# Kernel optimization log

Measured on AMD Instinct MI355X. Metric: run time of the kernel, lower is better.

## Reference

```python
import jax, jax.numpy as jnp
import numpy as np

B, S, D, H = 2, 2048, 1024, 16
HD = D // H  # 64
SCALE = float(np.sqrt(HD))


def setup_inputs() -> dict:
    key = jax.random.key(0)
    ks = jax.random.split(key, 5)
    x = jax.random.normal(ks[0], (B, S, D), dtype=jnp.float32)
    # causal mask: 1 = attend, 0 = masked
    mask = jnp.tril(jnp.ones((S, S), dtype=jnp.int32))
    xavier = lambda k: jax.random.normal(k, (D, D), dtype=jnp.float32) * np.sqrt(2.0 / (D + D))
    return {
        "x": x,
        "mask": mask,
        "Wq": xavier(ks[1]),
        "Wk": xavier(ks[2]),
        "Wv": xavier(ks[3]),
        "Wo": xavier(ks[4]),
    }


def reference(x, mask, Wq, Wk, Wv, Wo):
    # torch Linear(bias=False): y = x @ W.T  with W of shape [out, in]
    def heads(W):
        return (x @ W.T).reshape(B, S, H, HD).transpose(0, 2, 1, 3)  # [B,H,S,HD]

    Q, K, V = heads(Wq), heads(Wk), heads(Wv)
    scores = jnp.einsum("bhqd,bhkd->bhqk", Q, K) / SCALE  # [B,H,S,S]
    scores = jnp.where(mask[None, None] == 0, -jnp.inf, scores)
    attn = jax.nn.softmax(scores, axis=-1)
    attn = jnp.where(jnp.isnan(attn), jnp.zeros_like(attn), attn)  # nan-fix for fully masked rows
    # dropout is identity in eval / p=0
    out = jnp.einsum("bhqk,bhkd->bhqd", attn, V)  # [B,H,S,HD]
    out = out.transpose(0, 2, 1, 3).reshape(B, S, D)
    return out @ Wo.T
```

## Files before the change

kernel.cpp:

```cpp
#include <hip/hip_runtime.h>


using bfx8 = __attribute__((ext_vector_type(8))) short;
using fx4  = __attribute__((ext_vector_type(4))) float;

#define NB 2
#define NS 2048
#define ND 1024
#define NH 16
#define NHD 64

__device__ __forceinline__ unsigned short f2bf(float f) {
  union { float f; unsigned u; } v; v.f = f;
  return (unsigned short)((v.u + 0x7fffu + ((v.u >> 16) & 1u)) >> 16);
}
__device__ __forceinline__ unsigned pk2(float a, float b) {
  return (unsigned)f2bf(a) | ((unsigned)f2bf(b) << 16);
}
__device__ __forceinline__ unsigned pkt(float a, float b) {
  union { float f; unsigned u; } ua, ub; ua.f = a; ub.f = b;
  return (ua.u >> 16) | (ub.u & 0xffff0000u);
}
__device__ __forceinline__ int vperm32(int k5) {
  return (((k5 & 15) >> 2) << 3) + (((k5 >> 4) & 1) << 2) + (k5 & 3);
}

#define GLD16(gp, lp) __builtin_amdgcn_global_load_lds( \
    (__attribute__((address_space(1))) void*)(gp),      \
    (__attribute__((address_space(3))) void*)(lp), 16, 0, 0)

__global__ __launch_bounds__(256)
void cvt_all(const float4* __restrict__ x,  const float4* __restrict__ wq,
             const float4* __restrict__ wk, const float4* __restrict__ wv,
             const float4* __restrict__ wo, unsigned short* __restrict__ dst) {
  const int NT4 = (NB * NS * ND) / 4, NW4 = (ND * ND) / 4;
  const int i = blockIdx.x * 256 + threadIdx.x;
  const float4* src;
  int off;
  if (i < NT4) {
    src = x; off = i;
  } else {
    const int k = i - NT4;
    const int seg = k / NW4;
    off = k - seg * NW4;
    src = (seg == 0) ? wq : (seg == 1) ? wk : (seg == 2) ? wv : wo;
  }
  float4 f = src[off];
  uint2 w;
  w.x = pk2(f.x, f.y);
  w.y = pk2(f.z, f.w);
  *(uint2*)(dst + (size_t)i * 4) = w;
}

__global__ __launch_bounds__(256)
void gemm_qkvT(const unsigned short* __restrict__ Wcat,
               const unsigned short* __restrict__ xb,
               unsigned short* __restrict__ Qb, unsigned short* __restrict__ Kb,
               unsigned short* __restrict__ Vt, float SCL) {
  __shared__ __attribute__((aligned(16))) unsigned short As[3][128 * 32];
  __shared__ __attribute__((aligned(16))) unsigned short Bs[3][128 * 32];
  const int t = threadIdx.x;
  const int lane = t & 63, wave = t >> 6;
  const int wr = wave >> 1, wc = wave & 1;
  const int r16 = lane & 15, quad = lane >> 4;
  const int n0 = blockIdx.x * 128;
  const int m0 = blockIdx.y * 128;
  const int KD = 1024;
  fx4 acc[4][4] = {};
  const int c0 = t, c1 = t + 256;
  const size_t a0 = (size_t)(n0 + (c0 >> 2)) * KD + (size_t)(((c0 & 3) ^ ((c0 >> 3) & 3)) * 8);
  const size_t a1 = (size_t)(n0 + (c1 >> 2)) * KD + (size_t)(((c1 & 3) ^ ((c1 >> 3) & 3)) * 8);
  const size_t b0 = (size_t)(m0 + (c0 >> 2)) * KD + (size_t)(((c0 & 3) ^ ((c0 >> 3) & 3)) * 8);
  const size_t b1 = (size_t)(m0 + (c1 >> 2)) * KD + (size_t)(((c1 & 3) ^ ((c1 >> 3) & 3)) * 8);

#define QKVT_STAGE(bi, kk) do {                      \
    GLD16(Wcat + a0 + (kk), &As[bi][c0 * 8]);        \
    GLD16(Wcat + a1 + (kk), &As[bi][c1 * 8]);        \
    GLD16(xb   + b0 + (kk), &Bs[bi][c0 * 8]);        \
    GLD16(xb   + b1 + (kk), &Bs[bi][c1 * 8]);        \
  } while (0)

  QKVT_STAGE(0, 0);
  QKVT_STAGE(1, 32);
  QKVT_STAGE(2, 64);
  const int swr = (quad ^ ((r16 >> 1) & 3)) * 8;
  int cur = 0;
  for (int k0 = 0; k0 < KD; k0 += 32) {
    asm volatile("s_waitcnt vmcnt(8)" ::: "memory");
    __builtin_amdgcn_s_barrier();
    bfx8 af[4], bfr[4];
#pragma unroll
    for (int ni = 0; ni < 4; ni++)
      af[ni] = *(const bfx8*)&As[cur][(wr * 64 + ni * 16 + r16) * 32 + swr];
#pragma unroll
    for (int mi = 0; mi < 4; mi++)
      bfr[mi] = *(const bfx8*)&Bs[cur][(wc * 64 + mi * 16 + r16) * 32 + swr];
#pragma unroll
    for (int ni = 0; ni < 4; ni++)
#pragma unroll
      for (int mi = 0; mi < 4; mi++)
        acc[ni][mi] = __builtin_amdgcn_mfma_f32_16x16x32_bf16(
            af[ni], bfr[mi], acc[ni][mi], 0, 0, 0);
    __builtin_amdgcn_s_barrier();
    int kn = k0 + 96;
    if (kn >= KD) kn = KD - 32;
    QKVT_STAGE(cur, kn);
    cur = (cur == 2) ? 0 : cur + 1;
  }
#undef QKVT_STAGE
#pragma unroll
  for (int ni = 0; ni < 4; ni++) {
#pragma unroll
    for (int mi = 0; mi < 4; mi++) {
      fx4 v = acc[ni][mi];
      const int n = n0 + wr * 64 + ni * 16 + quad * 4;
      const int m = m0 + wc * 64 + mi * 16 + r16;
      const int b = m >> 11, s = m & (NS - 1);
      if (n0 < 1024) {
        const int h = n >> 6, hd = n & (NHD - 1);
        const size_t base = ((size_t)(b * NH + h) * NS + s) * NHD + hd;
        uint2 pw;
        pw.x = pk2(v[0] * SCL, v[1] * SCL);
        pw.y = pk2(v[2] * SCL, v[3] * SCL);
        *(uint2*)(Qb + base) = pw;
      } else if (n0 < 2048) {
        const int n2 = n - 1024;
        const int h = n2 >> 6, hd = n2 & (NHD - 1);
        const size_t base = ((size_t)(b * NH + h) * NS + s) * NHD + hd;
        uint2 pw;
        pw.x = pk2(v[0], v[1]);
        pw.y = pk2(v[2], v[3]);
        *(uint2*)(Kb + base) = pw;
      } else {
        const int n2 = n - 2048;
        const int h = n2 >> 6, hd = n2 & (NHD - 1);
        const int sp = (s & ~31) | vperm32(s & 31);
        const size_t base = ((size_t)(b * NH + h) * NHD + hd) * NS + sp;
#pragma unroll
        for (int r = 0; r < 4; r++) Vt[base + (size_t)r * NS] = f2bf(v[r]);
      }
    }
  }
}

__global__ __launch_bounds__(256)
void gemm_qkv_f32(const float* __restrict__ x,
                  const float* __restrict__ W0, const float* __restrict__ W1,
                  const float* __restrict__ W2,
                  unsigned short* __restrict__ Qb, unsigned short* __restrict__ Kb,
                  unsigned short* __restrict__ Vt, float SCL) {
  __shared__ __attribute__((aligned(16))) unsigned short As[128 * 32];
  __shared__ __attribute__((aligned(16))) unsigned short Bs[128 * 32];
  const int t = threadIdx.x;
  const int lane = t & 63, wave = t >> 6;
  const int wr = wave >> 1, wc = wave & 1;
  const int r16 = lane & 15, quad = lane >> 4;
  const int m0 = blockIdx.x * 128, n0 = blockIdx.y * 128;
  const int z = blockIdx.z;
  const float* W = (z == 0) ? W0 : (z == 1) ? W1 : W2;
  const int KD = 1024;
  fx4 acc[4][4] = {};
  const int row2 = t >> 1, kh = t & 1;
  for (int k0 = 0; k0 < KD; k0 += 32) {
    {
      const float4* src = (const float4*)(x + (size_t)(m0 + row2) * KD + k0 + kh * 16);
      float4 f0 = src[0], f1 = src[1], f2 = src[2], f3 = src[3];
      uint4 w0 = {pk2(f0.x, f0.y), pk2(f0.z, f0.w), pk2(f1.x, f1.y), pk2(f1.z, f1.w)};
      uint4 w1 = {pk2(f2.x, f2.y), pk2(f2.z, f2.w), pk2(f3.x, f3.y), pk2(f3.z, f3.w)};
      *(uint4*)&As[row2 * 32 + kh * 16] = w0;
      *(uint4*)&As[row2 * 32 + kh * 16 + 8] = w1;
    }
    {
      const float4* src = (const float4*)(W + (size_t)(n0 + row2) * KD + k0 + kh * 16);
      float4 f0 = src[0], f1 = src[1], f2 = src[2], f3 = src[3];
      uint4 w0 = {pk2(f0.x, f0.y), pk2(f0.z, f0.w), pk2(f1.x, f1.y), pk2(f1.z, f1.w)};
      uint4 w1 = {pk2(f2.x, f2.y), pk2(f2.z, f2.w), pk2(f3.x, f3.y), pk2(f3.z, f3.w)};
      *(uint4*)&Bs[row2 * 32 + kh * 16] = w0;
      *(uint4*)&Bs[row2 * 32 + kh * 16 + 8] = w1;
    }
    __syncthreads();
    bfx8 af[4], bfr[4];
#pragma unroll
    for (int mt = 0; mt < 4; mt++)
      af[mt] = *(const bfx8*)&As[(wr * 64 + mt * 16 + r16) * 32 + quad * 8];
#pragma unroll
    for (int nt = 0; nt < 4; nt++)
      bfr[nt] = *(const bfx8*)&Bs[(wc * 64 + nt * 16 + r16) * 32 + quad * 8];
#pragma unroll
    for (int mt = 0; mt < 4; mt++)
#pragma unroll
      for (int nt = 0; nt < 4; nt++)
        acc[mt][nt] = __builtin_amdgcn_mfma_f32_16x16x32_bf16(
            af[mt], bfr[nt], acc[mt][nt], 0, 0, 0);
    __syncthreads();
  }
#pragma unroll
  for (int mt = 0; mt < 4; mt++) {
#pragma unroll
    for (int nt = 0; nt < 4; nt++) {
      fx4 v = acc[mt][nt];
      const int mb = m0 + wr * 64 + mt * 16 + quad * 4;
      const int n = n0 + wc * 64 + nt * 16 + r16;
      const int b = mb >> 11, s = mb & (NS - 1);
      const int h = n >> 6, hd = n & (NHD - 1);
      if (z <= 1) {
        unsigned short* C = (z == 0) ? Qb : Kb;
        const float sc = (z == 0) ? SCL : 1.0f;
        const size_t base = ((size_t)(b * NH + h) * NS + s) * NHD + hd;
#pragma unroll
        for (int r = 0; r < 4; r++) C[base + (size_t)r * NHD] = f2bf(v[r] * sc);
      } else {
        const int sp = (s & ~31) | (((s & 15) >> 2) << 3) | (((s >> 4) & 1) << 2);
        const size_t base = ((size_t)(b * NH + h) * NHD + hd) * NS + sp;
        uint2 pw;
        pw.x = pk2(v[0], v[1]);
        pw.y = pk2(v[2], v[3]);
        *(uint2*)(Vt + base) = pw;
      }
    }
  }
}

template <bool BF16>
__global__ __launch_bounds__(256)
void gemm_out(const unsigned short* __restrict__ A,
              const void* __restrict__ Wv,
              float* __restrict__ C) {
  __shared__ __attribute__((aligned(16))) unsigned short As[64 * 64];
  __shared__ __attribute__((aligned(16))) unsigned short Bs[128 * 64];
  const int t = threadIdx.x;
  const int lane = t & 63, wave = t >> 6;
  const int wr = wave >> 1, wc = wave & 1;
  const int r16 = lane & 15, quad = lane >> 4;
  const int m0 = blockIdx.x * 64, n0 = blockIdx.y * 128;
  const int KD = 1024;
  fx4 acc[2][4] = {};
  for (int k0 = 0; k0 < KD; k0 += 64) {
#pragma unroll
    for (int cc = 0; cc < 2; cc++) {
      const int c = t + cc * 256;
      GLD16(A + (size_t)(m0 + (c >> 3)) * KD + (size_t)(((c & 7) ^ ((c >> 3) & 7)) * 8) + k0,
            &As[c * 8]);
    }
    if constexpr (BF16) {
      const unsigned short* W = (const unsigned short*)Wv;
#pragma unroll
      for (int cc = 0; cc < 4; cc++) {
        const int c = t + cc * 256;
        GLD16(W + (size_t)(n0 + (c >> 3)) * KD + (size_t)(((c & 7) ^ ((c >> 3) & 7)) * 8) + k0,
              &Bs[c * 8]);
      }
    } else {
      const float* W = (const float*)Wv;
#pragma unroll
      for (int cc = 0; cc < 4; cc++) {
        const int c = t + cc * 256;
        const float4* src = (const float4*)(W + (size_t)(n0 + (c >> 3)) * KD +
                                            ((c & 7) ^ ((c >> 3) & 7)) * 8 + k0);
        float4 f0 = src[0], f1 = src[1];
        uint4 w0 = {pk2(f0.x, f0.y), pk2(f0.z, f0.w), pk2(f1.x, f1.y), pk2(f1.z, f1.w)};
        *(uint4*)&Bs[c * 8] = w0;
      }
    }
    __syncthreads();
    bfx8 af[2][2], bfr[4][2];
#pragma unroll
    for (int ks = 0; ks < 2; ks++) {
      const int sw = ((ks * 4 + quad) ^ (r16 & 7)) * 8;
#pragma unroll
      for (int mt = 0; mt < 2; mt++)
        af[mt][ks] = *(const bfx8*)&As[(wr * 32 + mt * 16 + r16) * 64 + sw];
#pragma unroll
      for (int nt = 0; nt < 4; nt++)
        bfr[nt][ks] = *(const bfx8*)&Bs[(wc * 64 + nt * 16 + r16) * 64 + sw];
    }
#pragma unroll
    for (int ks = 0; ks < 2; ks++)
#pragma unroll
      for (int mt = 0; mt < 2; mt++)
#pragma unroll
        for (int nt = 0; nt < 4; nt++)
          acc[mt][nt] = __builtin_amdgcn_mfma_f32_16x16x32_bf16(
              af[mt][ks], bfr[nt][ks], acc[mt][nt], 0, 0, 0);
    __syncthreads();
  }
#pragma unroll
  for (int mt = 0; mt < 2; mt++) {
#pragma unroll
    for (int nt = 0; nt < 4; nt++) {
      fx4 v = acc[mt][nt];
      const int s = m0 + wr * 32 + mt * 16 + quad * 4;
      const int n = n0 + wc * 64 + nt * 16 + r16;
      const size_t base = (size_t)s * ND + n;
#pragma unroll
      for (int r = 0; r < 4; r++) C[base + (size_t)r * ND] = v[r];
    }
  }
}

__global__ __launch_bounds__(256)
void attn_mfma(const unsigned short* __restrict__ Q,
               const unsigned short* __restrict__ K,
               const unsigned short* __restrict__ Vt,
               unsigned short* __restrict__ O) {
  __shared__ __attribute__((aligned(16))) unsigned short Ks[64 * 64];
  __shared__ __attribute__((aligned(16))) unsigned short Vs[64 * 64];
  const int t = threadIdx.x;
  const int lane = t & 63, wave = t >> 6;
  const int r16 = lane & 15, quad = lane >> 4;
  const int bh = blockIdx.x;
  const int tile = (gridDim.y - 1) - blockIdx.y;
  const int b = bh >> 4, h = bh & (NH - 1);
  const int q0b = tile * 64;
  const int qbase = q0b + r16 * 4 + wave;
  const int nT = tile + 1;
  const unsigned short* Qp = Q + (size_t)bh * NS * NHD;
  const unsigned short* Kp = K + (size_t)bh * NS * NHD;
  const unsigned short* Vp = Vt + (size_t)bh * NHD * NS;

  bfx8 qf[2];
#pragma unroll
  for (int hs = 0; hs < 2; hs++)
    qf[hs] = *(const bfx8*)&Qp[(size_t)qbase * NHD + hs * 32 + quad * 8];

  fx4 acc[4] = {};
  float lsum = 0.0f;

  const int c0 = t, c1 = t + 256;
  const int ls0 = (c0 >> 3) * 64 + (((c0 & 7) ^ ((c0 >> 3) & 7)) * 8);
  const int ls1 = (c1 >> 3) * 64 + (((c1 & 7) ^ ((c1 >> 3) & 7)) * 8);
  const int rx = r16 & 7;
  uint4 kr0 = *(const uint4*)&Kp[8 * c0];
  uint4 kr1 = *(const uint4*)&Kp[8 * c1];
  uint4 vr0 = *(const uint4*)&Vp[(size_t)(c0 >> 3) * NS + (c0 & 7) * 8];
  uint4 vr1 = *(const uint4*)&Vp[(size_t)(c1 >> 3) * NS + (c1 & 7) * 8];

  for (int tt = 0; tt < nT; tt++) {
    __syncthreads();
    *(uint4*)&Ks[ls0] = kr0;
    *(uint4*)&Ks[ls1] = kr1;
    *(uint4*)&Vs[ls0] = vr0;
    *(uint4*)&Vs[ls1] = vr1;
    if (tt + 1 < nT) {
      const int kk = (tt + 1) * 64;
      kr0 = *(const uint4*)&Kp[kk * 64 + 8 * c0];
      kr1 = *(const uint4*)&Kp[kk * 64 + 8 * c1];
      vr0 = *(const uint4*)&Vp[(size_t)(c0 >> 3) * NS + kk + (c0 & 7) * 8];
      vr1 = *(const uint4*)&Vp[(size_t)(c1 >> 3) * NS + kk + (c1 & 7) * 8];
    }
    __syncthreads();

#pragma unroll
    for (int ks32 = 0; ks32 < 2; ks32++) {
      const int kkeff = tt * 64 + ks32 * 32;
      bfx8 kf[2][2];
      bfx8 vf[4];
#pragma unroll
      for (int kt = 0; kt < 2; kt++)
#pragma unroll
        for (int hs = 0; hs < 2; hs++)
          kf[kt][hs] = *(const bfx8*)&Ks[(ks32 * 32 + kt * 16 + r16) * 64 +
                                         (((hs * 4 + quad) ^ rx) * 8)];
#pragma unroll
      for (int mt = 0; mt < 4; mt++)
        vf[mt] = *(const bfx8*)&Vs[(mt * 16 + r16) * 64 +
                                   (((ks32 * 4 + quad) ^ rx) * 8)];

      fx4 st[2] = {};
      __builtin_amdgcn_s_setprio(1);
#pragma unroll
      for (int kt = 0; kt < 2; kt++)
#pragma unroll
        for (int hs = 0; hs < 2; hs++)
          st[kt] = __builtin_amdgcn_mfma_f32_16x16x32_bf16(
              kf[kt][hs], qf[hs], st[kt], 0, 0, 0);
      __builtin_amdgcn_s_setprio(0);

      if (kkeff >= q0b) {
#pragma unroll
        for (int kt = 0; kt < 2; kt++)
#pragma unroll
          for (int r = 0; r < 4; r++) {
            const int key = kkeff + kt * 16 + quad * 4 + r;
            if (key > qbase) st[kt][r] = -1e30f;
          }
      }

      float p[2][4];
      float ps = 0.0f;
#pragma unroll
      for (int kt = 0; kt < 2; kt++)
#pragma unroll
        for (int r = 0; r < 4; r++) {
          p[kt][r] = __builtin_amdgcn_exp2f(st[kt][r]);
          ps += p[kt][r];
        }
      lsum += ps;
      uint4 pbu;
      pbu.x = pkt(p[0][0], p[0][1]);
      pbu.y = pkt(p[0][2], p[0][3]);
      pbu.z = pkt(p[1][0], p[1][1]);
      pbu.w = pkt(p[1][2], p[1][3]);
      bfx8 pb = *(bfx8*)&pbu;
      __builtin_amdgcn_s_setprio(1);
#pragma unroll
      for (int mt = 0; mt < 4; mt++)
        acc[mt] = __builtin_amdgcn_mfma_f32_16x16x32_bf16(
            vf[mt], pb, acc[mt], 0, 0, 0);
      __builtin_amdgcn_s_setprio(0);
    }
  }

  {
    float l = lsum;
    l += __shfl_xor(l, 16);
    l += __shfl_xor(l, 32);
    const float rinv = 1.0f / l;
    const int s = qbase;
#pragma unroll
    for (int mt = 0; mt < 4; mt++) {
      const int d = h * NHD + mt * 16 + quad * 4;
      uint2 pw;
      pw.x = pk2(acc[mt][0] * rinv, acc[mt][1] * rinv);
      pw.y = pk2(acc[mt][2] * rinv, acc[mt][3] * rinv);
      *(uint2*)(O + ((size_t)b * NS + s) * ND + d) = pw;
    }
  }
}

extern "C" void kernel_launch(void* const* d_in, const int* in_sizes, int n_in,
                              void* d_out, int out_size, void* d_ws, size_t ws_size,
                              hipStream_t stream) {
  const float* x  = (const float*)d_in[0];
  const float* Wq = (const float*)d_in[2];
  const float* Wk = (const float*)d_in[3];
  const float* Wv = (const float*)d_in[4];
  const float* Wo = (const float*)d_in[5];
  float* out = (float*)d_out;
  unsigned short* ws = (unsigned short*)d_ws;
  const float QSCL = 0.125f * 1.44269504f;
  dim3 blk(256);
  const size_t NT = (size_t)NB * NS * ND;
  const size_t NW = (size_t)ND * ND;

  if (ws_size >= (size_t)48 * 1024 * 1024) {
    unsigned short* xb   = ws;
    unsigned short* Wcat = ws + NT;
    unsigned short* Wob  = ws + NT + 3 * NW;
    unsigned short* Qb   = ws + NT + 4 * NW;
    unsigned short* Kb   = Qb + NT;
    unsigned short* Vt   = Qb + 2 * NT;
    unsigned short* Ob   = Qb + 3 * NT;
    const int total4 = (int)((NT + 4 * NW) / 4);
    hipLaunchKernelGGL(cvt_all, dim3(total4 / 256), blk, 0, stream,
                       (const float4*)x, (const float4*)Wq, (const float4*)Wk,
                       (const float4*)Wv, (const float4*)Wo, xb);
    hipLaunchKernelGGL(gemm_qkvT, dim3(24, 32), blk, 0, stream,
                       Wcat, xb, Qb, Kb, Vt, QSCL);
    hipLaunchKernelGGL(attn_mfma, dim3(32, 32), blk, 0, stream, Qb, Kb, Vt, Ob);
    hipLaunchKernelGGL((gemm_out<true>), dim3(64, 8), blk, 0, stream, Ob, Wob, out);
  } else if (ws_size >= (size_t)32 * 1024 * 1024) {
    unsigned short* Qb = ws;
    unsigned short* Kb = ws + NT;
    unsigned short* Vt = ws + 2 * NT;
    unsigned short* Ob = ws + 3 * NT;
    hipLaunchKernelGGL(gemm_qkv_f32, dim3(32, 8, 3), blk, 0, stream,
                       x, Wq, Wk, Wv, Qb, Kb, Vt, QSCL);
    hipLaunchKernelGGL(attn_mfma, dim3(32, 32), blk, 0, stream, Qb, Kb, Vt, Ob);
    hipLaunchKernelGGL((gemm_out<false>), dim3(64, 8), blk, 0, stream, Ob, Wo, out);
  } else {
    const size_t NBA = (size_t)NS * ND;
    unsigned short* Qb = ws;
    unsigned short* Kb = ws + NBA;
    unsigned short* Vt = ws + 2 * NBA;
    unsigned short* Ob = ws + 3 * NBA;
    for (int b = 0; b < NB; b++) {
      const float* xb = x + (size_t)b * NS * ND;
      float* ob = out + (size_t)b * NS * ND;
      hipLaunchKernelGGL(gemm_qkv_f32, dim3(16, 8, 3), blk, 0, stream,
                         xb, Wq, Wk, Wv, Qb, Kb, Vt, QSCL);
      hipLaunchKernelGGL(attn_mfma, dim3(16, 32), blk, 0, stream, Qb, Kb, Vt, Ob);
      hipLaunchKernelGGL((gemm_out<false>), dim3(32, 8), blk, 0, stream, Ob, Wo, ob);
    }
  }
}
```

Measured before the change: 176.0 us.

## Load QKV GEMM fragments directly from global memory, dropping LDS pipeline

Removes the triple-buffered LDS staging (async global-to-LDS loads, swizzle, barriers) in the QKV projection GEMM and has each wave read its MFMA operand fragments straight from global memory, with the loop unrolled by two. This cuts the LDS traffic and barrier synchronisation and frees shared memory for higher occupancy. The trade-off is that the two waves sharing a tile row each fetch the same data, so operand reuse now depends on L1/L2 caching. Each lane's 16-byte loads are also strided across rows, which loses the coalescing and latency hiding the prefetch pipeline gave.

```diff
diff --git a/kernel.cpp b/kernel.cpp
--- a/kernel.cpp
+++ b/kernel.cpp
@@ -57,8 +57,6 @@
                const unsigned short* __restrict__ xb,
                unsigned short* __restrict__ Qb, unsigned short* __restrict__ Kb,
                unsigned short* __restrict__ Vt, float SCL) {
-  __shared__ __attribute__((aligned(16))) unsigned short As[3][128 * 32];
-  __shared__ __attribute__((aligned(16))) unsigned short Bs[3][128 * 32];
   const int t = threadIdx.x;
   const int lane = t & 63, wave = t >> 6;
   const int wr = wave >> 1, wc = wave & 1;
@@ -67,47 +65,25 @@
   const int m0 = blockIdx.y * 128;
   const int KD = 1024;
   fx4 acc[4][4] = {};
-  const int c0 = t, c1 = t + 256;
-  const size_t a0 = (size_t)(n0 + (c0 >> 2)) * KD + (size_t)(((c0 & 3) ^ ((c0 >> 3) & 3)) * 8);
-  const size_t a1 = (size_t)(n0 + (c1 >> 2)) * KD + (size_t)(((c1 & 3) ^ ((c1 >> 3) & 3)) * 8);
-  const size_t b0 = (size_t)(m0 + (c0 >> 2)) * KD + (size_t)(((c0 & 3) ^ ((c0 >> 3) & 3)) * 8);
-  const size_t b1 = (size_t)(m0 + (c1 >> 2)) * KD + (size_t)(((c1 & 3) ^ ((c1 >> 3) & 3)) * 8);
-
-#define QKVT_STAGE(bi, kk) do {                      \
-    GLD16(Wcat + a0 + (kk), &As[bi][c0 * 8]);        \
-    GLD16(Wcat + a1 + (kk), &As[bi][c1 * 8]);        \
-    GLD16(xb   + b0 + (kk), &Bs[bi][c0 * 8]);        \
-    GLD16(xb   + b1 + (kk), &Bs[bi][c1 * 8]);        \
-  } while (0)
-
-  QKVT_STAGE(0, 0);
-  QKVT_STAGE(1, 32);
-  QKVT_STAGE(2, 64);
-  const int swr = (quad ^ ((r16 >> 1) & 3)) * 8;
-  int cur = 0;
+  const unsigned short* pA = Wcat + (size_t)(n0 + wr * 64 + r16) * KD + quad * 8;
+  const unsigned short* pB = xb   + (size_t)(m0 + wc * 64 + r16) * KD + quad * 8;
+
+#pragma unroll 2
   for (int k0 = 0; k0 < KD; k0 += 32) {
-    asm volatile("s_waitcnt vmcnt(8)" ::: "memory");
-    __builtin_amdgcn_s_barrier();
     bfx8 af[4], bfr[4];
 #pragma unroll
     for (int ni = 0; ni < 4; ni++)
-      af[ni] = *(const bfx8*)&As[cur][(wr * 64 + ni * 16 + r16) * 32 + swr];
+      af[ni] = *(const bfx8*)(pA + (size_t)ni * 16 * KD + k0);
 #pragma unroll
     for (int mi = 0; mi < 4; mi++)
-      bfr[mi] = *(const bfx8*)&Bs[cur][(wc * 64 + mi * 16 + r16) * 32 + swr];
+      bfr[mi] = *(const bfx8*)(pB + (size_t)mi * 16 * KD + k0);
 #pragma unroll
     for (int ni = 0; ni < 4; ni++)
 #pragma unroll
       for (int mi = 0; mi < 4; mi++)
         acc[ni][mi] = __builtin_amdgcn_mfma_f32_16x16x32_bf16(
             af[ni], bfr[mi], acc[ni][mi], 0, 0, 0);
-    __builtin_amdgcn_s_barrier();
-    int kn = k0 + 96;
-    if (kn >= KD) kn = KD - 32;
-    QKVT_STAGE(cur, kn);
-    cur = (cur == 2) ? 0 : cur + 1;
-  }
-#undef QKVT_STAGE
+  }
 #pragma unroll
   for (int ni = 0; ni < 4; ni++) {
 #pragma unroll
```

Result: slower. 256.8 us (+45.9%).
